# Kernel tuning notes

Hardware: AMD Instinct MI355X
Metric: run time of the kernel (lower is better)

## Reference

```python
import jax, jax.numpy as jnp
import numpy as np

D_MODEL = 1024
NUM_HEADS = 16
D_HEAD = D_MODEL // NUM_HEADS
LN_EPS = 1e-5
ROPE_BASE = 10000.0


def layer_norm(x, w, b=None, eps=LN_EPS):
    mu = jnp.mean(x, axis=-1, keepdims=True)
    var = jnp.mean(jnp.square(x - mu), axis=-1, keepdims=True)
    y = (x - mu) * jax.lax.rsqrt(var + eps) * w
    return y + b if b is not None else y


def _rotate_half(x):
    x1, x2 = jnp.split(x, 2, axis=-1)
    return jnp.concatenate([-x2, x1], axis=-1)


def apply_rotary(q, k):
    # q, k: [B, S, H, Dh]
    s, dh = q.shape[1], q.shape[-1]
    inv_freq = 1.0 / (ROPE_BASE ** (jnp.arange(0, dh, 2, dtype=jnp.float32) / dh))
    t = jnp.arange(s, dtype=jnp.float32)
    freqs = jnp.outer(t, inv_freq)                      # [S, Dh/2]
    emb = jnp.concatenate([freqs, freqs], axis=-1)      # [S, Dh]
    cos = jnp.cos(emb)[None, :, None, :].astype(q.dtype)
    sin = jnp.sin(emb)[None, :, None, :].astype(q.dtype)
    q_rot = q * cos + _rotate_half(q) * sin
    k_rot = k * cos + _rotate_half(k) * sin
    return q_rot, k_rot


def setup_inputs() -> dict:
    key = jax.random.key(0)
    ks = jax.random.split(key, 8)
    B, L, D = 4, 2048, D_MODEL
    x = jax.random.normal(ks[0], (B, L, D), dtype=jnp.float32)
    sequence_id = jnp.sort(jax.random.randint(ks[1], (B, L), 0, 8), axis=-1).astype(jnp.int64)
    scale = 1.0 / np.sqrt(D)
    return {
        "x": x,
        "sequence_id": sequence_id,
        "ln_w": jnp.ones((D,), jnp.float32),
        "ln_b": jnp.zeros((D,), jnp.float32),
        "w_qkv": jax.random.normal(ks[2], (D, 3 * D), jnp.float32) * scale,
        "q_ln_w": jnp.ones((D,), jnp.float32),
        "k_ln_w": jnp.ones((D,), jnp.float32),
        "w_out": jax.random.normal(ks[3], (D, D), jnp.float32) * scale,
    }


def reference(x, sequence_id, ln_w, ln_b, w_qkv, q_ln_w, k_ln_w, w_out):
    B, L, D = x.shape
    H, Dh = NUM_HEADS, D_HEAD
    # fused LayerNorm + QKV projection
    qkv = layer_norm(x, ln_w, ln_b) @ w_qkv              # [B, L, 3D]
    q, k, v = jnp.split(qkv, 3, axis=-1)
    # qk layernorm (scale only, bias=False)
    q = layer_norm(q, q_ln_w)
    k = layer_norm(k, k_ln_w)
    # split heads and apply rotary
    q = q.reshape(B, L, H, Dh)
    k = k.reshape(B, L, H, Dh)
    q, k = apply_rotary(q, k)
    v = v.reshape(B, L, H, Dh)
    # packed-sequence mask: tokens attend only within same sequence id
    mask = (sequence_id[:, :, None] == sequence_id[:, None, :])[:, None, :, :]  # [B,1,L,L]
    scale = 1.0 / np.sqrt(Dh)
    scores = jnp.einsum("bqhd,bkhd->bhqk", q, k) * scale
    scores = jnp.where(mask, scores, jnp.finfo(scores.dtype).min)
    attn = jax.nn.softmax(scores, axis=-1)
    ctx = jnp.einsum("bhqk,bkhd->bqhd", attn, v).reshape(B, L, D)
    return ctx @ w_out
```

## Files before the change

kernel.cpp:

```cpp
#include <hip/hip_runtime.h>
#include <hip/hip_bf16.h>
#include <cstdint>
#include <cstddef>
#include <type_traits>

#define D_MODEL 1024
#define NH      16
#define DH      64
#define LSEQ    2048
#define BATCH   4
#define NTOK    8192
#define K3      3072

typedef __attribute__((ext_vector_type(8))) short  short8;
typedef __attribute__((ext_vector_type(4))) float  floatx4;

__device__ __forceinline__ unsigned short f2bf_bits(float f) {
  __hip_bfloat16 h = __float2bfloat16(f);
  return __builtin_bit_cast(unsigned short, h);
}
__device__ __forceinline__ float bf2f(unsigned short u) {
  return __bfloat162float(__builtin_bit_cast(__hip_bfloat16, u));
}
__device__ __forceinline__ unsigned int pack_bf16(float lo, float hi) {
  return (unsigned int)f2bf_bits(lo) | ((unsigned int)f2bf_bits(hi) << 16);
}

__device__ __forceinline__ void gld_lds16(const void* g, void* l) {
  __builtin_amdgcn_global_load_lds(
      (const __attribute__((address_space(1))) void*)g,
      (__attribute__((address_space(3))) void*)l,
      16, 0, 0);
}

__global__ __launch_bounds__(256)
void prep_kernel(const float* __restrict__ x, const float* __restrict__ ln_w,
                 const float* __restrict__ ln_b, const float* __restrict__ w_qkv,
                 const float* __restrict__ w_out, const int* __restrict__ sid,
                 __hip_bfloat16* __restrict__ hbuf, __hip_bfloat16* __restrict__ wqkvT,
                 __hip_bfloat16* __restrict__ woutT, int* __restrict__ segstart,
                 int* __restrict__ segend) {
  __shared__ __align__(16) char smem[8448];
  const int blk = blockIdx.x;
  const int tid = threadIdx.x;

  if (blk < 4096) {
    float (*tile)[33] = reinterpret_cast<float(*)[33]>(smem);
    const float* src;  __hip_bfloat16* dst;  int R, C, bx, by;
    if (blk < 3072) { src = w_qkv; dst = wqkvT; R = 1024; C = 3072; bx = blk % 96; by = blk / 96; }
    else            { src = w_out; dst = woutT; R = 1024; C = 1024; bx = (blk - 3072) & 31; by = (blk - 3072) >> 5; }
    const int c0 = bx * 32, r0 = by * 32;
    const int xx = tid & 31, yy = tid >> 5;
    #pragma unroll
    for (int j = 0; j < 32; j += 8)
      tile[yy + j][xx] = src[(size_t)(r0 + yy + j) * C + c0 + xx];
    __syncthreads();
    #pragma unroll
    for (int j = 0; j < 32; j += 8)
      dst[(size_t)(c0 + yy + j) * R + r0 + xx] = __float2bfloat16(tile[xx][yy + j]);
  } else if (blk < 6144) {
    const int lane = tid & 63;
    const int t = (blk - 4096) * 4 + (tid >> 6);
    const float4* xr = reinterpret_cast<const float4*>(x) + (size_t)t * 256;
    float4 v[4];
    float s = 0.f, ss = 0.f;
    #pragma unroll
    for (int i = 0; i < 4; i++) {
      v[i] = xr[lane + i * 64];
      s  += (v[i].x + v[i].y) + (v[i].z + v[i].w);
      ss += (v[i].x*v[i].x + v[i].y*v[i].y) + (v[i].z*v[i].z + v[i].w*v[i].w);
    }
    #pragma unroll
    for (int off = 1; off < 64; off <<= 1) {
      s  += __shfl_xor(s, off);
      ss += __shfl_xor(ss, off);
    }
    const float mu = s * (1.f / 1024);
    const float rs = rsqrtf(ss * (1.f / 1024) - mu * mu + 1e-5f);
    const float4* wr = reinterpret_cast<const float4*>(ln_w);
    const float4* br = reinterpret_cast<const float4*>(ln_b);
    ushort4* hr = reinterpret_cast<ushort4*>(hbuf) + (size_t)t * 256;
    #pragma unroll
    for (int i = 0; i < 4; i++) {
      const float4 wv = wr[lane + i * 64];
      const float4 bv = br[lane + i * 64];
      ushort4 o;
      o.x = f2bf_bits((v[i].x - mu) * rs * wv.x + bv.x);
      o.y = f2bf_bits((v[i].y - mu) * rs * wv.y + bv.y);
      o.z = f2bf_bits((v[i].z - mu) * rs * wv.z + bv.z);
      o.w = f2bf_bits((v[i].w - mu) * rs * wv.w + bv.w);
      hr[lane + i * 64] = o;
    }
  } else {
    int* srow = reinterpret_cast<int*>(smem);
    const int sblk = blk - 6144;
    const int b = sblk >> 3;
    const int* row = sid + (size_t)b * LSEQ;
    #pragma unroll
    for (int i = 0; i < 8; i++) srow[tid + i * 256] = row[tid + i * 256];
    __syncthreads();
    const int l = (sblk & 7) * 256 + tid;
    const int v = srow[l];
    int lo = 0, hi = l;
    while (lo < hi) { int mid = (lo + hi) >> 1; if (srow[mid] < v) lo = mid + 1; else hi = mid; }
    const int i = b * LSEQ + l;
    segstart[i] = lo;
    lo = l + 1; hi = LSEQ;
    while (lo < hi) { int mid = (lo + hi) >> 1; if (srow[mid] <= v) lo = mid + 1; else hi = mid; }
    segend[i] = lo;
  }
}

template <typename OutT>
__global__ __launch_bounds__(256, 2)
void gemm_bt(const __hip_bfloat16* __restrict__ A, const __hip_bfloat16* __restrict__ Bt,
             OutT* __restrict__ C, int M, int N, int K) {
  const int tid  = threadIdx.x;
  const int lane = tid & 63;
  const int wave = tid >> 6;
  const int bm = blockIdx.y * 128;
  const int bn = blockIdx.x * 128;
  const int wm = (wave & 1) * 64;
  const int wn = (wave >> 1) * 64;
  const int quad = lane >> 4;
  const int l16  = lane & 15;

  __shared__ __align__(16) __hip_bfloat16 As[128 * 64];
  __shared__ __align__(16) __hip_bfloat16 Bs[128 * 64];

  floatx4 acc[4][4];
  #pragma unroll
  for (int i = 0; i < 4; i++)
    #pragma unroll
    for (int j = 0; j < 4; j++) {
      floatx4 z = {0.f, 0.f, 0.f, 0.f};
      acc[i][j] = z;
    }

  const int srow = tid >> 3;
  const int sq   = tid & 7;
  const int sc8  = (sq ^ (srow & 7)) * 8;
  const __hip_bfloat16* Ab = A  + (size_t)(bm + srow) * K + sc8;
  const __hip_bfloat16* Bb = Bt + (size_t)(bn + srow) * K + sc8;

  const int axr = l16 & 7;

  for (int k0 = 0; k0 < K; k0 += 64) {
    __syncthreads();
    #pragma unroll
    for (int p = 0; p < 4; p++) {
      gld_lds16(Ab + (size_t)(p * 32) * K + k0, (char*)As + p * 4096 + tid * 16);
      gld_lds16(Bb + (size_t)(p * 32) * K + k0, (char*)Bs + p * 4096 + tid * 16);
    }
    __syncthreads();
    #pragma unroll
    for (int s0 = 0; s0 < 2; s0++) {
      const int qo = ((s0 * 4 + quad) ^ axr) * 8;
      short8 af[4], bfr[4];
      #pragma unroll
      for (int i = 0; i < 4; i++)
        af[i] = *reinterpret_cast<const short8*>(As + (wm + i * 16 + l16) * 64 + qo);
      #pragma unroll
      for (int j = 0; j < 4; j++)
        bfr[j] = *reinterpret_cast<const short8*>(Bs + (wn + j * 16 + l16) * 64 + qo);
      #pragma unroll
      for (int i = 0; i < 4; i++)
        #pragma unroll
        for (int j = 0; j < 4; j++)
          acc[i][j] = __builtin_amdgcn_mfma_f32_16x16x32_bf16(af[i], bfr[j], acc[i][j], 0, 0, 0);
    }
  }

  #pragma unroll
  for (int i = 0; i < 4; i++)
    #pragma unroll
    for (int j = 0; j < 4; j++) {
      const int row0 = bm + wm + i * 16 + quad * 4;
      const int col  = bn + wn + j * 16 + l16;
      #pragma unroll
      for (int r = 0; r < 4; r++) {
        if constexpr (std::is_same<OutT, __hip_bfloat16>::value)
          C[(size_t)(row0 + r) * N + col] = __float2bfloat16(acc[i][j][r]);
        else
          C[(size_t)(row0 + r) * N + col] = acc[i][j][r];
      }
    }
}

__global__ __launch_bounds__(256)
void ropevt_kernel(const unsigned short* __restrict__ qkv, const float* __restrict__ qw,
                   const float* __restrict__ kw, unsigned short* __restrict__ qT,
                   unsigned short* __restrict__ kT, unsigned short* __restrict__ vT) {
  __shared__ __align__(16) unsigned short T[64 * 64];
  const int blk = blockIdx.x;
  const int tid = threadIdx.x;

  if (blk < 2048) {
    const int lane = tid & 63;
    const int t = blk * 4 + (tid >> 6);
    const int b = t >> 11, l = t & 2047;
    const unsigned short* row = qkv + (size_t)t * K3;
    const int hh = lane >> 2;
    const int jb = (lane & 3) * 8;
    const int base = hh * 64 + jb;

    const short8 qa_u = *reinterpret_cast<const short8*>(row + base);
    const short8 qb_u = *reinterpret_cast<const short8*>(row + base + 32);
    const short8 ka_u = *reinterpret_cast<const short8*>(row + 1024 + base);
    const short8 kb_u = *reinterpret_cast<const short8*>(row + 1024 + base + 32);

    float qa[8], qb[8], ka[8], kb[8];
    float s_q = 0.f, ss_q = 0.f, s_k = 0.f, ss_k = 0.f;
    #pragma unroll
    for (int e = 0; e < 8; e++) {
      qa[e] = bf2f((unsigned short)qa_u[e]); qb[e] = bf2f((unsigned short)qb_u[e]);
      ka[e] = bf2f((unsigned short)ka_u[e]); kb[e] = bf2f((unsigned short)kb_u[e]);
      s_q  += qa[e] + qb[e];  ss_q += qa[e]*qa[e] + qb[e]*qb[e];
      s_k  += ka[e] + kb[e];  ss_k += ka[e]*ka[e] + kb[e]*kb[e];
    }
    #pragma unroll
    for (int off = 1; off < 64; off <<= 1) {
      s_q  += __shfl_xor(s_q, off);  ss_q += __shfl_xor(ss_q, off);
      s_k  += __shfl_xor(s_k, off);  ss_k += __shfl_xor(ss_k, off);
    }
    const float qmu = s_q * (1.f/1024);
    const float qrs = rsqrtf(ss_q * (1.f/1024) - qmu*qmu + 1e-5f);
    const float kmu = s_k * (1.f/1024);
    const float krs = rsqrtf(ss_k * (1.f/1024) - kmu*kmu + 1e-5f);

    const int j0 = lane & 31;
    const float invf = __expf(-(float)j0 * 0.28782313662425575f);
    float tsin, tcos;
    sincosf((float)l * invf, &tsin, &tcos);

    const float4 wq0 = *reinterpret_cast<const float4*>(qw + base);
    const float4 wq1 = *reinterpret_cast<const float4*>(qw + base + 4);
    const float4 wq2 = *reinterpret_cast<const float4*>(qw + base + 32);
    const float4 wq3 = *reinterpret_cast<const float4*>(qw + base + 36);
    const float4 wk0 = *reinterpret_cast<const float4*>(kw + base);
    const float4 wk1 = *reinterpret_cast<const float4*>(kw + base + 4);
    const float4 wk2 = *reinterpret_cast<const float4*>(kw + base + 32);
    const float4 wk3 = *reinterpret_cast<const float4*>(kw + base + 36);
    const float wqa[8] = {wq0.x,wq0.y,wq0.z,wq0.w, wq1.x,wq1.y,wq1.z,wq1.w};
    const float wqb[8] = {wq2.x,wq2.y,wq2.z,wq2.w, wq3.x,wq3.y,wq3.z,wq3.w};
    const float wka[8] = {wk0.x,wk0.y,wk0.z,wk0.w, wk1.x,wk1.y,wk1.z,wk1.w};
    const float wkb[8] = {wk2.x,wk2.y,wk2.z,wk2.w, wk3.x,wk3.y,wk3.z,wk3.w};

    short8 oqa, oqb, oka, okb;
    #pragma unroll
    for (int e = 0; e < 8; e++) {
      const int j = jb + e;
      const float c  = __shfl(tcos, j);
      const float sn = __shfl(tsin, j);
      const float qn1 = (qa[e] - qmu) * qrs * wqa[e];
      const float qn2 = (qb[e] - qmu) * qrs * wqb[e];
      const float kn1 = (ka[e] - kmu) * krs * wka[e];
      const float kn2 = (kb[e] - kmu) * krs * wkb[e];
      oqa[e] = (short)f2bf_bits((qn1 * c - qn2 * sn) * 0.125f);
      oqb[e] = (short)f2bf_bits((qn2 * c + qn1 * sn) * 0.125f);
      oka[e] = (short)f2bf_bits(kn1 * c - kn2 * sn);
      okb[e] = (short)f2bf_bits(kn2 * c + kn1 * sn);
    }
    const size_t ob = ((size_t)(b * NH + hh) * LSEQ + l) * DH + jb;
    *reinterpret_cast<short8*>(qT + ob)      = oqa;
    *reinterpret_cast<short8*>(qT + ob + 32) = oqb;
    *reinterpret_cast<short8*>(kT + ob)      = oka;
    *reinterpret_cast<short8*>(kT + ob + 32) = okb;
  } else {
    const int blkv = blk - 2048;
    const int l0 = (blkv & 31) * 64;
    const int bh = blkv >> 5;
    const int b = bh >> 4, h = bh & 15;
    const int sr = tid >> 3, scc = tid & 7;
    const int r1 = sr + 32;
    gld_lds16(qkv + (size_t)(b * LSEQ + l0 + sr) * K3 + 2048 + h * 64 + ((scc ^ ((sr >> 3) & 7)) * 8),
              (char*)T + tid * 16);
    gld_lds16(qkv + (size_t)(b * LSEQ + l0 + r1) * K3 + 2048 + h * 64 + ((scc ^ ((r1 >> 3) & 7)) * 8),
              (char*)T + 4096 + tid * 16);
    __syncthreads();
    #pragma unroll
    for (int it = 0; it < 2; it++) {
      const int cid = tid + it * 256;
      const int dh = cid >> 3, c = (cid & 7) * 8;
      const int sl = (dh >> 3) ^ ((c >> 3) & 7);
      short8 o;
      #pragma unroll
      for (int e = 0; e < 8; e++)
        o[e] = (short)T[(c + e) * 64 + sl * 8 + (dh & 7)];
      *reinterpret_cast<short8*>(vT + ((size_t)bh * DH + dh) * LSEQ + l0 + c) = o;
    }
  }
}

__global__ __launch_bounds__(256)
void attn_mfma(const unsigned short* __restrict__ qT, const unsigned short* __restrict__ kT,
               const unsigned short* __restrict__ vT, const int* __restrict__ segs,
               const int* __restrict__ sege, unsigned short* __restrict__ ctx) {
  const int tid  = threadIdx.x;
  const int lane = tid & 63, w = tid >> 6;
  const int quad = lane >> 4, l16 = lane & 15;
  const int qbase = blockIdx.x * 128;
  const int h = blockIdx.y, b = blockIdx.z;
  const size_t bh = (size_t)(b * NH + h);
  const unsigned short* Kg = kT + bh * LSEQ * DH;
  const unsigned short* Vg = vT + bh * DH * LSEQ;

  __shared__ __align__(16) unsigned short Ks[64 * 72];
  __shared__ __align__(16) unsigned short Vs[64 * 72];
  __shared__ __align__(16) unsigned short Ps[4][32 * 72];

  short8 qf[2][2];
  int st[2], en[2];
  #pragma unroll
  for (int g = 0; g < 2; g++) {
    const int qy = qbase + w * 32 + g * 16 + l16;
    const unsigned short* Qrow = qT + (bh * LSEQ + qy) * DH;
    qf[g][0] = *reinterpret_cast<const short8*>(Qrow + quad * 8);
    qf[g][1] = *reinterpret_cast<const short8*>(Qrow + 32 + quad * 8);
    st[g] = segs[b * LSEQ + qy];
    en[g] = sege[b * LSEQ + qy];
  }

  const int kmin = segs[b * LSEQ + qbase] & ~63;
  const int kmax = sege[b * LSEQ + qbase + 127];
  const int wmin = segs[b * LSEQ + qbase + w * 32];
  const int wmax = sege[b * LSEQ + qbase + w * 32 + 31];
  int gmin[2], gmax[2];
  #pragma unroll
  for (int g = 0; g < 2; g++) {
    gmin[g] = segs[b * LSEQ + qbase + w * 32 + g * 16];
    gmax[g] = sege[b * LSEQ + qbase + w * 32 + g * 16 + 15];
  }

  floatx4 acc[2][4];
  #pragma unroll
  for (int g = 0; g < 2; g++)
    #pragma unroll
    for (int dt = 0; dt < 4; dt++) { floatx4 z = {0.f,0.f,0.f,0.f}; acc[g][dt] = z; }
  float m[2] = {-1e30f, -1e30f}, lsum[2] = {0.f, 0.f};

  const int r_ = tid >> 3, c_ = (tid & 7) * 8;

  for (int kk = kmin; kk < kmax; kk += 64) {
    __syncthreads();
    #pragma unroll
    for (int it = 0; it < 2; it++) {
      const int r = r_ + it * 32;
      *reinterpret_cast<short8*>(Ks + r * 72 + c_) =
          *reinterpret_cast<const short8*>(Kg + (size_t)(kk + r) * DH + c_);
      *reinterpret_cast<short8*>(Vs + r * 72 + c_) =
          *reinterpret_cast<const short8*>(Vg + (size_t)r * LSEQ + kk + c_);
    }
    __syncthreads();

    if (kk + 64 <= wmin || kk >= wmax) continue;

    float alpha[2];
    bool act[2];
    #pragma unroll
    for (int g = 0; g < 2; g++) {
      act[g] = !(kk + 64 <= gmin[g] || kk >= gmax[g]);
      alpha[g] = 1.f;
      if (!act[g]) continue;

      floatx4 sc[4];
      #pragma unroll
      for (int t = 0; t < 4; t++) {
        const short8 kf0 = *reinterpret_cast<const short8*>(Ks + (t * 16 + l16) * 72 + quad * 8);
        const short8 kf1 = *reinterpret_cast<const short8*>(Ks + (t * 16 + l16) * 72 + 32 + quad * 8);
        floatx4 z = {0.f,0.f,0.f,0.f};
        sc[t] = __builtin_amdgcn_mfma_f32_16x16x32_bf16(kf0, qf[g][0], z, 0, 0, 0);
        sc[t] = __builtin_amdgcn_mfma_f32_16x16x32_bf16(kf1, qf[g][1], sc[t], 0, 0, 0);
      }

      const unsigned span = (unsigned)(en[g] - st[g]);
      float vm = -1e30f;
      #pragma unroll
      for (int t = 0; t < 4; t++) {
        const int k0 = kk + t * 16 + quad * 4;
        #pragma unroll
        for (int r = 0; r < 4; r++) {
          const bool ok = (unsigned)(k0 + r - st[g]) < span;
          sc[t][r] = ok ? sc[t][r] : -1e30f;
          vm = fmaxf(vm, sc[t][r]);
        }
      }
      vm = fmaxf(vm, __shfl_xor(vm, 16));
      vm = fmaxf(vm, __shfl_xor(vm, 32));
      const float mn = fmaxf(m[g], vm);
      alpha[g] = __expf(m[g] - mn);
      m[g] = mn;

      float rs = 0.f;
      #pragma unroll
      for (int t = 0; t < 4; t++) {
        float p0 = (sc[t][0] > -1e29f) ? __expf(sc[t][0] - mn) : 0.f;
        float p1 = (sc[t][1] > -1e29f) ? __expf(sc[t][1] - mn) : 0.f;
        float p2 = (sc[t][2] > -1e29f) ? __expf(sc[t][2] - mn) : 0.f;
        float p3 = (sc[t][3] > -1e29f) ? __expf(sc[t][3] - mn) : 0.f;
        rs += (p0 + p1) + (p2 + p3);
        uint2 pk;
        pk.x = pack_bf16(p0, p1);
        pk.y = pack_bf16(p2, p3);
        *reinterpret_cast<uint2*>(&Ps[w][(g * 16 + l16) * 72 + t * 16 + quad * 4]) = pk;
      }
      rs += __shfl_xor(rs, 16);
      rs += __shfl_xor(rs, 32);
      lsum[g] = lsum[g] * alpha[g] + rs;
    }

    short8 pf[2][2];
    #pragma unroll
    for (int g = 0; g < 2; g++) {
      if (!act[g]) continue;
      pf[g][0] = *reinterpret_cast<const short8*>(&Ps[w][(g * 16 + l16) * 72 + quad * 8]);
      pf[g][1] = *reinterpret_cast<const short8*>(&Ps[w][(g * 16 + l16) * 72 + 32 + quad * 8]);
    }
    #pragma unroll
    for (int dt = 0; dt < 4; dt++) {
      const short8 vf0 = *reinterpret_cast<const short8*>(Vs + (dt * 16 + l16) * 72 + quad * 8);
      const short8 vf1 = *reinterpret_cast<const short8*>(Vs + (dt * 16 + l16) * 72 + 32 + quad * 8);
      #pragma unroll
      for (int g = 0; g < 2; g++) {
        if (!act[g]) continue;
        #pragma unroll
        for (int r = 0; r < 4; r++) acc[g][dt][r] *= alpha[g];
        acc[g][dt] = __builtin_amdgcn_mfma_f32_16x16x32_bf16(vf0, pf[g][0], acc[g][dt], 0, 0, 0);
        acc[g][dt] = __builtin_amdgcn_mfma_f32_16x16x32_bf16(vf1, pf[g][1], acc[g][dt], 0, 0, 0);
      }
    }
  }

  #pragma unroll
  for (int g = 0; g < 2; g++) {
    const float inv = (lsum[g] > 0.f) ? 1.f / lsum[g] : 0.f;
    const int qy = qbase + w * 32 + g * 16 + l16;
    unsigned short* orow = ctx + ((size_t)(b * LSEQ + qy)) * D_MODEL + h * DH;
    #pragma unroll
    for (int dt = 0; dt < 4; dt++) {
      uint2 o;
      o.x = pack_bf16(acc[g][dt][0] * inv, acc[g][dt][1] * inv);
      o.y = pack_bf16(acc[g][dt][2] * inv, acc[g][dt][3] * inv);
      *reinterpret_cast<uint2*>(orow + dt * 16 + quad * 4) = o;
    }
  }
}

extern "C" void kernel_launch(void* const* d_in, const int* in_sizes, int n_in,
                              void* d_out, int out_size, void* d_ws, size_t ws_size,
                              hipStream_t stream) {
  const float* x      = (const float*)d_in[0];
  const int*   sid    = (const int*)d_in[1];
  const float* ln_w   = (const float*)d_in[2];
  const float* ln_b   = (const float*)d_in[3];
  const float* w_qkv  = (const float*)d_in[4];
  const float* q_ln_w = (const float*)d_in[5];
  const float* k_ln_w = (const float*)d_in[6];
  const float* w_out  = (const float*)d_in[7];
  float* out = (float*)d_out;
  char* ws = (char*)d_ws;

  constexpr size_t OFF_WQKVT = 0;
  constexpr size_t OFF_WOUTT = 6291456;
  constexpr size_t OFF_H     = 8388608;
  constexpr size_t OFF_QKV   = 25165824;
  constexpr size_t OFF_QT    = 75497472;
  constexpr size_t OFF_KT    = 92274688;
  constexpr size_t OFF_VT    = 109051904;
  constexpr size_t OFF_CTX   = 125829120;
  constexpr size_t OFF_SEGS  = 142606336;
  constexpr size_t OFF_SEGE  = 142639104;

  __hip_bfloat16* wqkvT = (__hip_bfloat16*)(ws + OFF_WQKVT);
  __hip_bfloat16* woutT = (__hip_bfloat16*)(ws + OFF_WOUTT);
  __hip_bfloat16* hbuf  = (__hip_bfloat16*)(ws + OFF_H);
  __hip_bfloat16* qkvb  = (__hip_bfloat16*)(ws + OFF_QKV);
  unsigned short* qTb   = (unsigned short*)(ws + OFF_QT);
  unsigned short* kTb   = (unsigned short*)(ws + OFF_KT);
  unsigned short* vTb   = (unsigned short*)(ws + OFF_VT);
  unsigned short* ctx   = (unsigned short*)(ws + OFF_CTX);
  int*            segst = (int*)(ws + OFF_SEGS);
  int*            segen = (int*)(ws + OFF_SEGE);

  prep_kernel<<<6176, 256, 0, stream>>>(x, ln_w, ln_b, w_qkv, w_out, sid,
                                        hbuf, wqkvT, woutT, segst, segen);
  gemm_bt<__hip_bfloat16><<<dim3(K3 / 128, NTOK / 128), 256, 0, stream>>>(
      hbuf, wqkvT, qkvb, NTOK, K3, 1024);
  ropevt_kernel<<<4096, 256, 0, stream>>>((const unsigned short*)qkvb, q_ln_w, k_ln_w,
                                          qTb, kTb, vTb);
  attn_mfma<<<dim3(LSEQ / 128, NH, BATCH), 256, 0, stream>>>(qTb, kTb, vTb, segst, segen, ctx);
  gemm_bt<float><<<dim3(D_MODEL / 128, NTOK / 128), 256, 0, stream>>>(
      (const __hip_bfloat16*)ctx, woutT, out, NTOK, D_MODEL, 1024);
}
```

Measured before the change: 250.1 us.

## Load K/V fragments directly from global memory and remap blocks for L2 locality

Removes the shared-memory K/V staging and both block-wide barriers in the attention loop. Each wave now reads its K and V MFMA fragments straight from global memory and only iterates over its own key range. The block index is also swizzled so that neighbouring workgroups land on different heads/batches, and launch bounds request 4 blocks per CU. The trade-off is that the four waves of a block no longer share K/V data, so global and L2 traffic per wave goes up, and the global loads are narrower than the old staged copies.

```diff
diff --git a/kernel.cpp b/kernel.cpp
--- a/kernel.cpp
+++ b/kernel.cpp
@@ -292,25 +292,27 @@
   }
 }
 
-__global__ __launch_bounds__(256)
+__global__ __launch_bounds__(256, 4)
 void attn_mfma(const unsigned short* __restrict__ qT, const unsigned short* __restrict__ kT,
                const unsigned short* __restrict__ vT, const int* __restrict__ segs,
                const int* __restrict__ sege, unsigned short* __restrict__ ctx) {
   const int tid  = threadIdx.x;
   const int lane = tid & 63, w = tid >> 6;
   const int quad = lane >> 4, l16 = lane & 15;
-  const int qbase = blockIdx.x * 128;
-  const int h = blockIdx.y, b = blockIdx.z;
+
+  const int fid = blockIdx.x + (blockIdx.y << 4) + (blockIdx.z << 8);
+  const int sw  = (fid & 7) * 128 + (fid >> 3);
+  const int qbase = (sw & 15) * 128;
+  const int h = (sw >> 4) & 15, b = sw >> 8;
+
   const size_t bh = (size_t)(b * NH + h);
   const unsigned short* Kg = kT + bh * LSEQ * DH;
   const unsigned short* Vg = vT + bh * DH * LSEQ;
 
-  __shared__ __align__(16) unsigned short Ks[64 * 72];
-  __shared__ __align__(16) unsigned short Vs[64 * 72];
   __shared__ __align__(16) unsigned short Ps[4][32 * 72];
 
   short8 qf[2][2];
-  int st[2], en[2];
+  int st[2], en[2], gmin[2], gmax[2];
   #pragma unroll
   for (int g = 0; g < 2; g++) {
     const int qy = qbase + w * 32 + g * 16 + l16;
@@ -319,18 +321,11 @@
     qf[g][1] = *reinterpret_cast<const short8*>(Qrow + 32 + quad * 8);
     st[g] = segs[b * LSEQ + qy];
     en[g] = sege[b * LSEQ + qy];
-  }
-
-  const int kmin = segs[b * LSEQ + qbase] & ~63;
-  const int kmax = sege[b * LSEQ + qbase + 127];
-  const int wmin = segs[b * LSEQ + qbase + w * 32];
-  const int wmax = sege[b * LSEQ + qbase + w * 32 + 31];
-  int gmin[2], gmax[2];
-  #pragma unroll
-  for (int g = 0; g < 2; g++) {
     gmin[g] = segs[b * LSEQ + qbase + w * 32 + g * 16];
     gmax[g] = sege[b * LSEQ + qbase + w * 32 + g * 16 + 15];
   }
+  const int wmin = gmin[0] & ~63;
+  const int wmax = gmax[1];
 
   floatx4 acc[2][4];
   #pragma unroll
@@ -339,40 +334,33 @@
     for (int dt = 0; dt < 4; dt++) { floatx4 z = {0.f,0.f,0.f,0.f}; acc[g][dt] = z; }
   float m[2] = {-1e30f, -1e30f}, lsum[2] = {0.f, 0.f};
 
-  const int r_ = tid >> 3, c_ = (tid & 7) * 8;
-
-  for (int kk = kmin; kk < kmax; kk += 64) {
-    __syncthreads();
-    #pragma unroll
-    for (int it = 0; it < 2; it++) {
-      const int r = r_ + it * 32;
-      *reinterpret_cast<short8*>(Ks + r * 72 + c_) =
-          *reinterpret_cast<const short8*>(Kg + (size_t)(kk + r) * DH + c_);
-      *reinterpret_cast<short8*>(Vs + r * 72 + c_) =
-          *reinterpret_cast<const short8*>(Vg + (size_t)r * LSEQ + kk + c_);
-    }
-    __syncthreads();
-
-    if (kk + 64 <= wmin || kk >= wmax) continue;
-
+  for (int kk = wmin; kk < wmax; kk += 64) {
+    bool act[2];
     float alpha[2];
-    bool act[2];
     #pragma unroll
     for (int g = 0; g < 2; g++) {
       act[g] = !(kk + 64 <= gmin[g] || kk >= gmax[g]);
       alpha[g] = 1.f;
+    }
+
+    floatx4 sc[2][4];
+    #pragma unroll
+    for (int t = 0; t < 4; t++) {
+      const unsigned short* kp = Kg + (size_t)(kk + t * 16 + l16) * DH + quad * 8;
+      const short8 kf0 = *reinterpret_cast<const short8*>(kp);
+      const short8 kf1 = *reinterpret_cast<const short8*>(kp + 32);
+      #pragma unroll
+      for (int g = 0; g < 2; g++) {
+        if (!act[g]) continue;
+        floatx4 z = {0.f,0.f,0.f,0.f};
+        sc[g][t] = __builtin_amdgcn_mfma_f32_16x16x32_bf16(kf0, qf[g][0], z, 0, 0, 0);
+        sc[g][t] = __builtin_amdgcn_mfma_f32_16x16x32_bf16(kf1, qf[g][1], sc[g][t], 0, 0, 0);
+      }
+    }
+
+    #pragma unroll
+    for (int g = 0; g < 2; g++) {
       if (!act[g]) continue;
-
-      floatx4 sc[4];
-      #pragma unroll
-      for (int t = 0; t < 4; t++) {
-        const short8 kf0 = *reinterpret_cast<const short8*>(Ks + (t * 16 + l16) * 72 + quad * 8);
-        const short8 kf1 = *reinterpret_cast<const short8*>(Ks + (t * 16 + l16) * 72 + 32 + quad * 8);
-        floatx4 z = {0.f,0.f,0.f,0.f};
-        sc[t] = __builtin_amdgcn_mfma_f32_16x16x32_bf16(kf0, qf[g][0], z, 0, 0, 0);
-        sc[t] = __builtin_amdgcn_mfma_f32_16x16x32_bf16(kf1, qf[g][1], sc[t], 0, 0, 0);
-      }
-
       const unsigned span = (unsigned)(en[g] - st[g]);
       float vm = -1e30f;
       #pragma unroll
@@ -381,8 +369,8 @@
         #pragma unroll
         for (int r = 0; r < 4; r++) {
           const bool ok = (unsigned)(k0 + r - st[g]) < span;
-          sc[t][r] = ok ? sc[t][r] : -1e30f;
-          vm = fmaxf(vm, sc[t][r]);
+          sc[g][t][r] = ok ? sc[g][t][r] : -1e30f;
+          vm = fmaxf(vm, sc[g][t][r]);
         }
       }
       vm = fmaxf(vm, __shfl_xor(vm, 16));
@@ -394,10 +382,10 @@
       float rs = 0.f;
       #pragma unroll
       for (int t = 0; t < 4; t++) {
-        float p0 = (sc[t][0] > -1e29f) ? __expf(sc[t][0] - mn) : 0.f;
-        float p1 = (sc[t][1] > -1e29f) ? __expf(sc[t][1] - mn) : 0.f;
-        float p2 = (sc[t][2] > -1e29f) ? __expf(sc[t][2] - mn) : 0.f;
-        float p3 = (sc[t][3] > -1e29f) ? __expf(sc[t][3] - mn) : 0.f;
+        float p0 = (sc[g][t][0] > -1e29f) ? __expf(sc[g][t][0] - mn) : 0.f;
+        float p1 = (sc[g][t][1] > -1e29f) ? __expf(sc[g][t][1] - mn) : 0.f;
+        float p2 = (sc[g][t][2] > -1e29f) ? __expf(sc[g][t][2] - mn) : 0.f;
+        float p3 = (sc[g][t][3] > -1e29f) ? __expf(sc[g][t][3] - mn) : 0.f;
         rs += (p0 + p1) + (p2 + p3);
         uint2 pk;
         pk.x = pack_bf16(p0, p1);
@@ -418,8 +406,9 @@
     }
     #pragma unroll
     for (int dt = 0; dt < 4; dt++) {
-      const short8 vf0 = *reinterpret_cast<const short8*>(Vs + (dt * 16 + l16) * 72 + quad * 8);
-      const short8 vf1 = *reinterpret_cast<const short8*>(Vs + (dt * 16 + l16) * 72 + 32 + quad * 8);
+      const unsigned short* vp = Vg + (size_t)(dt * 16 + l16) * LSEQ + kk + quad * 8;
+      const short8 vf0 = *reinterpret_cast<const short8*>(vp);
+      const short8 vf1 = *reinterpret_cast<const short8*>(vp + 32);
       #pragma unroll
       for (int g = 0; g < 2; g++) {
         if (!act[g]) continue;
```

Result: slower. 294.2 us (+17.7%).
